# Kernel optimization log

Measured on AMD Instinct MI355X. Metric: run time of the kernel, lower is better.

## Reference

```python
import jax, jax.numpy as jnp
import numpy as np

N, E = 50000, 800000
IN_C, HID, OUT_C, HEADS = 768, 64, 8, 8
NEG_SLOPE = 0.2
BN_EPS = 1e-5


def _bn(x, g, b, m, v):
    # BatchNorm1d in eval mode with running stats
    return (x - m) * jax.lax.rsqrt(v + BN_EPS) * g + b


def _gat_conv(x, W, att_src, att_dst, bias, src, dst, n):
    H, C = att_src.shape
    xw = (x @ W).reshape(n, H, C)                      # [N,H,C]
    a_src = jnp.sum(xw * att_src, axis=-1)             # [N,H]
    a_dst = jnp.sum(xw * att_dst, axis=-1)             # [N,H]
    alpha = jax.nn.leaky_relu(a_src[src] + a_dst[dst], NEG_SLOPE)  # [E',H]
    amax = jax.ops.segment_max(alpha, dst, num_segments=n)          # [N,H]
    ex = jnp.exp(alpha - amax[dst])
    denom = jax.ops.segment_sum(ex, dst, num_segments=n)            # [N,H]
    coef = ex / denom[dst]                                          # [E',H]
    out = jax.ops.segment_sum(xw[src] * coef[:, :, None], dst, num_segments=n)
    return out.reshape(n, H * C) + bias


def setup_inputs() -> dict:
    key = jax.random.key(0)
    ks = jax.random.split(key, 24)
    d = {}
    d['x'] = jax.random.normal(ks[0], (N, IN_C), dtype=jnp.float32)
    d['edge_index'] = jax.random.randint(ks[1], (2, E), 0, N, dtype=jnp.int32)
    d['proj_W'] = jax.random.normal(ks[2], (IN_C, HID), dtype=jnp.float32) * (IN_C ** -0.5)
    d['proj_b'] = jnp.zeros((HID,), jnp.float32)
    for i, kb in zip((1, 2, 3), (ks[3], ks[4], ks[5])):
        k1, k2 = jax.random.split(kb)
        d[f'bn{i}_g'] = jnp.ones((HID,), jnp.float32)
        d[f'bn{i}_b'] = jnp.zeros((HID,), jnp.float32)
        d[f'bn{i}_m'] = jax.random.normal(k1, (HID,), dtype=jnp.float32) * 0.1
        d[f'bn{i}_v'] = jax.random.uniform(k2, (HID,), dtype=jnp.float32, minval=0.5, maxval=1.5)
    C1 = HID // HEADS
    d['W1'] = jax.random.normal(ks[6], (HID, HEADS * C1), dtype=jnp.float32) * (HID ** -0.5)
    d['att_src1'] = jax.random.normal(ks[7], (HEADS, C1), dtype=jnp.float32) * 0.1
    d['att_dst1'] = jax.random.normal(ks[8], (HEADS, C1), dtype=jnp.float32) * 0.1
    d['b1'] = jnp.zeros((HEADS * C1,), jnp.float32)
    d['W2'] = jax.random.normal(ks[9], (HID, HID), dtype=jnp.float32) * (HID ** -0.5)
    d['att_src2'] = jax.random.normal(ks[10], (1, HID), dtype=jnp.float32) * 0.1
    d['att_dst2'] = jax.random.normal(ks[11], (1, HID), dtype=jnp.float32) * 0.1
    d['b2'] = jnp.zeros((HID,), jnp.float32)
    d['cls_W'] = jax.random.normal(ks[12], (HID, OUT_C), dtype=jnp.float32) * (HID ** -0.5)
    d['cls_b'] = jnp.zeros((OUT_C,), jnp.float32)
    return d


def reference(x, edge_index, proj_W, proj_b,
              bn1_g, bn1_b, bn1_m, bn1_v,
              W1, att_src1, att_dst1, b1,
              bn2_g, bn2_b, bn2_m, bn2_v,
              W2, att_src2, att_dst2, b2,
              bn3_g, bn3_b, bn3_m, bn3_v,
              cls_W, cls_b):
    n = x.shape[0]
    # add self-loops (PyG GATConv default)
    loop = jnp.arange(n, dtype=edge_index.dtype)
    src = jnp.concatenate([edge_index[0], loop])
    dst = jnp.concatenate([edge_index[1], loop])

    h = x @ proj_W + proj_b
    h = jax.nn.elu(_bn(h, bn1_g, bn1_b, bn1_m, bn1_v))
    identity = h
    h = _gat_conv(h, W1, att_src1, att_dst1, b1, src, dst, n)
    h = jax.nn.elu(_bn(h, bn2_g, bn2_b, bn2_m, bn2_v) + identity)
    identity = h
    h = _gat_conv(h, W2, att_src2, att_dst2, b2, src, dst, n)
    h = jax.nn.elu(_bn(h, bn3_g, bn3_b, bn3_m, bn3_v) + identity)
    return h @ cls_W + cls_b
```

## Files before the change

### kernel.cpp

```cpp
#include <hip/hip_runtime.h>

typedef __bf16 bf16;
typedef __attribute__((ext_vector_type(8))) __bf16 bf16x8;
typedef __attribute__((ext_vector_type(4))) __bf16 bf16x4;
typedef __attribute__((ext_vector_type(4))) float f32x4;
typedef unsigned short u16;

#define LSTR  40
#define LSTR2 72
#define BN_EPS 1e-5f

__device__ inline float bfl(unsigned int w) { return __uint_as_float(w << 16); }
__device__ inline float bfh(unsigned int w) { return __uint_as_float(w & 0xffff0000u); }

__global__ __launch_bounds__(256) void k_prep(
        const float* __restrict__ W0, const float* __restrict__ W1, const float* __restrict__ W2,
        bf16* __restrict__ Wt0, bf16* __restrict__ Wt1, bf16* __restrict__ Wt2,
        int* __restrict__ cnt, int n)
{
    int i = blockIdx.x*256 + threadIdx.x;
    const int T = 768*64 + 8192;
    if (i < 768*64)            { int k = i>>6, n_ = i&63;                  Wt0[n_*768+k] = (bf16)W0[i]; }
    else if (i < 768*64+4096)  { int j = i-768*64;      int k=j>>6,c=j&63; Wt1[c*64+k]  = (bf16)W1[j]; }
    else if (i < T)            { int j = i-768*64-4096; int k=j>>6,c=j&63; Wt2[c*64+k]  = (bf16)W2[j]; }
    int j = i - T;
    if (j >= 0 && j < n) cnt[j] = 0;
}

__global__ __launch_bounds__(256) void k_fused_proj(
        const float* __restrict__ A, const bf16* __restrict__ Bt,
        const bf16* __restrict__ W1t, int M,
        const float* __restrict__ pb, const float* __restrict__ g,
        const float* __restrict__ bb, const float* __restrict__ mm, const float* __restrict__ vv,
        const float* __restrict__ att_s, const float* __restrict__ att_d,
        bf16* __restrict__ h0b, bf16* __restrict__ xwb,
        float* __restrict__ a_s, float* __restrict__ a_d)
{
    const int K = 768;
    __shared__ bf16 xs[2][64*LSTR];
    __shared__ bf16 bs[2][64*LSTR];
    __shared__ bf16 hs [64*LSTR2];
    __shared__ bf16 w1s[64*LSTR2];
    __shared__ float sC[64], cC[64];

    int t = threadIdx.x;
    int w = t >> 6, lane = t & 63;
    int q = lane >> 4, l16 = lane & 15;
    int row0 = blockIdx.x * 64;
    int sRow = t >> 2, sK = (t & 3) * 8;

    if (t < 64) {
        float s = rsqrtf(vv[t] + BN_EPS) * g[t];
        sC[t] = s;
        cC[t] = (pb[t] - mm[t]) * s + bb[t];
    }
    {
        int r = t >> 2, c0 = (t & 3) * 16;
        *(bf16x8*)(w1s + r*LSTR2 + c0)     = *(const bf16x8*)(W1t + r*64 + c0);
        *(bf16x8*)(w1s + r*LSTR2 + c0 + 8) = *(const bf16x8*)(W1t + r*64 + c0 + 8);
    }

    auto loadA = [&](int k0) -> bf16x8 {
        bf16x8 xv;
        #pragma unroll
        for (int i = 0; i < 8; ++i) xv[i] = (bf16)0.f;
        int gr = row0 + sRow;
        if (gr < M) {
            const float* ap = A + (size_t)gr*K + k0 + sK;
            float4 f0 = *(const float4*)ap;
            float4 f1 = *(const float4*)(ap + 4);
            xv[0]=(bf16)f0.x; xv[1]=(bf16)f0.y; xv[2]=(bf16)f0.z; xv[3]=(bf16)f0.w;
            xv[4]=(bf16)f1.x; xv[5]=(bf16)f1.y; xv[6]=(bf16)f1.z; xv[7]=(bf16)f1.w;
        }
        return xv;
    };
    auto loadB = [&](int k0) -> bf16x8 {
        return *(const bf16x8*)(Bt + (size_t)sRow*K + k0 + sK);
    };

    f32x4 acc[4];
    #pragma unroll
    for (int i = 0; i < 4; ++i) { acc[i][0]=0.f; acc[i][1]=0.f; acc[i][2]=0.f; acc[i][3]=0.f; }

    bf16x8 xv = loadA(0);
    bf16x8 bv = loadB(0);
    *(bf16x8*)(&xs[0][sRow*LSTR + sK]) = xv;
    *(bf16x8*)(&bs[0][sRow*LSTR + sK]) = bv;
    __syncthreads();

    int cur = 0;
    for (int k0 = 0; k0 < K; k0 += 32) {
        if (k0 + 32 < K) {
            xv = loadA(k0 + 32);
            bv = loadB(k0 + 32);
        }
        bf16x8 af = *(bf16x8*)(&xs[cur][(w*16 + l16)*LSTR + q*8]);
        #pragma unroll
        for (int tt = 0; tt < 4; ++tt) {
            bf16x8 bfr = *(bf16x8*)(&bs[cur][(tt*16 + l16)*LSTR + q*8]);
            acc[tt] = __builtin_amdgcn_mfma_f32_16x16x32_bf16(af, bfr, acc[tt], 0, 0, 0);
        }
        if (k0 + 32 < K) {
            *(bf16x8*)(&xs[cur^1][sRow*LSTR + sK]) = xv;
            *(bf16x8*)(&bs[cur^1][sRow*LSTR + sK]) = bv;
            __syncthreads();
            cur ^= 1;
        }
    }

    #pragma unroll
    for (int tt = 0; tt < 4; ++tt) {
        int col = tt*16 + l16;
        #pragma unroll
        for (int r = 0; r < 4; ++r) {
            int rl = w*16 + q*4 + r;
            float val = acc[tt][r] * sC[col] + cC[col];
            val = val > 0.f ? val : __expf(val) - 1.f;
            hs[rl*LSTR2 + col] = (bf16)val;
            int row = row0 + rl;
            if (row < M) h0b[(size_t)row*64 + col] = (bf16)val;
        }
    }
    __syncthreads();

    f32x4 acc2[4];
    #pragma unroll
    for (int i = 0; i < 4; ++i) { acc2[i][0]=0.f; acc2[i][1]=0.f; acc2[i][2]=0.f; acc2[i][3]=0.f; }
    #pragma unroll
    for (int ks = 0; ks < 2; ++ks) {
        bf16x8 af = *(bf16x8*)(&hs[(w*16 + l16)*LSTR2 + ks*32 + q*8]);
        #pragma unroll
        for (int tt = 0; tt < 4; ++tt) {
            bf16x8 bfr = *(bf16x8*)(&w1s[(tt*16 + l16)*LSTR2 + ks*32 + q*8]);
            acc2[tt] = __builtin_amdgcn_mfma_f32_16x16x32_bf16(af, bfr, acc2[tt], 0, 0, 0);
        }
    }

    #pragma unroll
    for (int tt = 0; tt < 4; ++tt) {
        int col = tt*16 + l16;
        #pragma unroll
        for (int r = 0; r < 4; ++r) {
            int row = row0 + w*16 + q*4 + r;
            if (row < M) xwb[(size_t)row*64 + col] = (bf16)acc2[tt][r];
        }
    }
    #pragma unroll
    for (int r = 0; r < 4; ++r) {
        int row = row0 + w*16 + q*4 + r;
        float ps[4], pd[4];
        #pragma unroll
        for (int tt = 0; tt < 4; ++tt) {
            int col = tt*16 + l16;
            ps[tt] = acc2[tt][r] * att_s[col];
            pd[tt] = acc2[tt][r] * att_d[col];
        }
        #pragma unroll
        for (int off = 1; off < 8; off <<= 1) {
            #pragma unroll
            for (int tt = 0; tt < 4; ++tt) {
                ps[tt] += __shfl_xor(ps[tt], off);
                pd[tt] += __shfl_xor(pd[tt], off);
            }
        }
        if ((l16 & 7) == 0 && row < M) {
            int hb = l16 >> 3;
            #pragma unroll
            for (int tt = 0; tt < 4; ++tt) {
                a_s[row*8 + 2*tt + hb] = ps[tt];
                a_d[row*8 + 2*tt + hb] = pd[tt];
            }
        }
    }
}

template<int MODE, bool ABF, int H>
__global__ __launch_bounds__(256) void k_gemm64(
        const void* __restrict__ Av, const bf16* __restrict__ Bt, int M, int K,
        const float* __restrict__ pb, const float* __restrict__ g, const float* __restrict__ bb,
        const float* __restrict__ mm, const float* __restrict__ vv,
        bf16* __restrict__ outB,
        float* __restrict__ a_s, float* __restrict__ a_d,
        const float* __restrict__ att_s, const float* __restrict__ att_d)
{
    __shared__ bf16 xs[64*LSTR];
    __shared__ bf16 bs[64*LSTR];
    __shared__ float sC[64], cC[64];

    int t = threadIdx.x;
    int w = t >> 6, lane = t & 63;
    int q = lane >> 4, l16 = lane & 15;
    int row0 = blockIdx.x * 64;
    int sRow = t >> 2, sK = (t & 3) * 8;

    auto loadA = [&](int k0) -> bf16x8 {
        bf16x8 xv;
        #pragma unroll
        for (int i = 0; i < 8; ++i) xv[i] = (bf16)0.f;
        int gr = row0 + sRow;
        if (gr < M) {
            if constexpr (ABF) {
                xv = *(const bf16x8*)((const bf16*)Av + (size_t)gr*K + k0 + sK);
            } else {
                const float* ap = (const float*)Av + (size_t)gr*K + k0 + sK;
                float4 f0 = *(const float4*)ap;
                float4 f1 = *(const float4*)(ap + 4);
                xv[0]=(bf16)f0.x; xv[1]=(bf16)f0.y; xv[2]=(bf16)f0.z; xv[3]=(bf16)f0.w;
                xv[4]=(bf16)f1.x; xv[5]=(bf16)f1.y; xv[6]=(bf16)f1.z; xv[7]=(bf16)f1.w;
            }
        }
        return xv;
    };
    auto loadB = [&](int k0) -> bf16x8 {
        return *(const bf16x8*)(Bt + (size_t)sRow*K + k0 + sK);
    };

    f32x4 acc[4];
    #pragma unroll
    for (int i = 0; i < 4; ++i) { acc[i][0]=0.f; acc[i][1]=0.f; acc[i][2]=0.f; acc[i][3]=0.f; }

    bf16x8 xv = loadA(0);
    bf16x8 bv = loadB(0);

    for (int k0 = 0; k0 < K; k0 += 32) {
        *(bf16x8*)(xs + sRow*LSTR + sK) = xv;
        *(bf16x8*)(bs + sRow*LSTR + sK) = bv;
        __syncthreads();
        if (k0 + 32 < K) {
            xv = loadA(k0 + 32);
            bv = loadB(k0 + 32);
        }
        bf16x8 af = *(bf16x8*)(xs + (w*16 + l16)*LSTR + q*8);
        #pragma unroll
        for (int tt = 0; tt < 4; ++tt) {
            bf16x8 bfr = *(bf16x8*)(bs + (tt*16 + l16)*LSTR + q*8);
            acc[tt] = __builtin_amdgcn_mfma_f32_16x16x32_bf16(af, bfr, acc[tt], 0, 0, 0);
        }
        __syncthreads();
    }

    if constexpr (MODE == 0) {
        if (t < 64) {
            float s = rsqrtf(vv[t] + BN_EPS) * g[t];
            sC[t] = s;
            cC[t] = (pb[t] - mm[t]) * s + bb[t];
        }
        __syncthreads();
    }

    #pragma unroll
    for (int tt = 0; tt < 4; ++tt) {
        int col = tt*16 + l16;
        #pragma unroll
        for (int r = 0; r < 4; ++r) {
            int row = row0 + w*16 + q*4 + r;
            if (row < M) {
                float val = acc[tt][r];
                if constexpr (MODE == 0) {
                    val = val * sC[col] + cC[col];
                    val = val > 0.f ? val : __expf(val) - 1.f;
                }
                outB[(size_t)row*64 + col] = (bf16)val;
            }
        }
    }

    if constexpr (MODE == 1) {
        #pragma unroll
        for (int r = 0; r < 4; ++r) {
            int row = row0 + w*16 + q*4 + r;
            if constexpr (H == 1) {
                float ps = 0.f, pd = 0.f;
                #pragma unroll
                for (int tt = 0; tt < 4; ++tt) {
                    int col = tt*16 + l16;
                    ps += acc[tt][r] * att_s[col];
                    pd += acc[tt][r] * att_d[col];
                }
                #pragma unroll
                for (int off = 1; off < 16; off <<= 1) {
                    ps += __shfl_xor(ps, off);
                    pd += __shfl_xor(pd, off);
                }
                if (l16 == 0 && row < M) { a_s[row] = ps; a_d[row] = pd; }
            } else {
                float ps[4], pd[4];
                #pragma unroll
                for (int tt = 0; tt < 4; ++tt) {
                    int col = tt*16 + l16;
                    ps[tt] = acc[tt][r] * att_s[col];
                    pd[tt] = acc[tt][r] * att_d[col];
                }
                #pragma unroll
                for (int off = 1; off < 8; off <<= 1) {
                    #pragma unroll
                    for (int tt = 0; tt < 4; ++tt) {
                        ps[tt] += __shfl_xor(ps[tt], off);
                        pd[tt] += __shfl_xor(pd[tt], off);
                    }
                }
                if ((l16 & 7) == 0 && row < M) {
                    int hb = l16 >> 3;
                    #pragma unroll
                    for (int tt = 0; tt < 4; ++tt) {
                        a_s[row*8 + 2*tt + hb] = ps[tt];
                        a_d[row*8 + 2*tt + hb] = pd[tt];
                    }
                }
            }
        }
    }
}

__global__ __launch_bounds__(256) void k_count(const int* __restrict__ dst, int E, int* cnt) {
    int i = blockIdx.x*256 + threadIdx.x;
    if (i < E) atomicAdd(&cnt[dst[i]], 1);
}
__global__ __launch_bounds__(256) void k_scan_block(const int* __restrict__ cnt,
        int* __restrict__ rp, int* __restrict__ bsum, int n) {
    __shared__ int s[256];
    int t = threadIdx.x, v = blockIdx.x*256 + t;
    int x = (v < n) ? cnt[v] : 0;
    s[t] = x; __syncthreads();
    for (int off = 1; off < 256; off <<= 1) {
        int y = (t >= off) ? s[t-off] : 0;
        __syncthreads();
        s[t] += y;
        __syncthreads();
    }
    if (v < n) rp[v+1] = s[t];
    if (t == 255) bsum[blockIdx.x] = s[255];
}
__global__ __launch_bounds__(256) void k_finalize(int* __restrict__ rp, const int* __restrict__ bsum,
        const int* __restrict__ cnt, int* __restrict__ cursor, int n, int nb) {
    __shared__ int s[256];
    int t = threadIdx.x;
    int x = (t < nb) ? bsum[t] : 0;
    s[t] = x; __syncthreads();
    for (int off = 1; off < 256; off <<= 1) {
        int y = (t >= off) ? s[t-off] : 0;
        __syncthreads();
        s[t] += y;
        __syncthreads();
    }
    int v = blockIdx.x*256 + t;
    if (v < n) {
        int b = v >> 8;
        int off0 = (b == 0) ? 0 : s[b-1];
        int val = rp[v+1] + off0;
        rp[v+1] = val;
        cursor[v] = val - cnt[v];
        if (v == 0) rp[0] = 0;
    }
}
__global__ __launch_bounds__(256) void k_scatter(const int* __restrict__ src, const int* __restrict__ dst,
        int E, int* __restrict__ cursor, u16* __restrict__ in_src) {
    int i = blockIdx.x*256 + threadIdx.x;
    if (i < E) {
        int pos = atomicAdd(&cursor[dst[i]], 1);
        in_src[pos] = (u16)src[i];
    }
}

template<int H, bool CLS>
__global__ __launch_bounds__(256) void k_gat_agg(const bf16* __restrict__ xwb,
        const float* __restrict__ a_src, const float* __restrict__ a_dst,
        const int* __restrict__ rp, const u16* __restrict__ in_src,
        const float* __restrict__ bias,
        const float* __restrict__ g_, const float* __restrict__ bb,
        const float* __restrict__ mm, const float* __restrict__ vv,
        const bf16* __restrict__ resid, bf16* __restrict__ outB, float* __restrict__ outF,
        const float* __restrict__ clsW, const float* __restrict__ clsb, int n)
{
    int wv = (blockIdx.x*256 + threadIdx.x) >> 6;
    int lane = threadIdx.x & 63;
    if (wv >= n) return;
    int eg = lane >> 4;
    int s  = lane & 15;
    int c0 = s * 4;
    int h  = (H == 8) ? (s >> 1) : 0;
    float adst = a_dst[(size_t)wv*H + h];

    float a0 = 0.f, a1 = 0.f, a2 = 0.f, a3 = 0.f, den = 0.f;

    if (eg == 0) {
        float asf = a_src[(size_t)wv*H + h] + adst;
        asf = (asf > 0.f) ? asf : 0.2f*asf;
        float ex = __expf(asf);
        uint2 xw = *(const uint2*)(xwb + (size_t)wv*64 + c0);
        a0 = ex*bfl(xw.x); a1 = ex*bfh(xw.x); a2 = ex*bfl(xw.y); a3 = ex*bfh(xw.y);
        den = ex;
    }

    int beg = rp[wv], end = rp[wv+1];
    int e = beg;
    for (; e + 8 <= end; e += 8) {
        int u0 = (int)in_src[e + eg];
        int u1 = (int)in_src[e + 4 + eg];
        float s0 = a_src[(size_t)u0*H + h];
        float s1 = a_src[(size_t)u1*H + h];
        uint2 x0 = *(const uint2*)(xwb + (size_t)u0*64 + c0);
        uint2 x1 = *(const uint2*)(xwb + (size_t)u1*64 + c0);
        float al0 = s0 + adst; al0 = (al0 > 0.f) ? al0 : 0.2f*al0;
        float al1 = s1 + adst; al1 = (al1 > 0.f) ? al1 : 0.2f*al1;
        float e0 = __expf(al0), e1 = __expf(al1);
        a0 += e0*bfl(x0.x) + e1*bfl(x1.x);
        a1 += e0*bfh(x0.x) + e1*bfh(x1.x);
        a2 += e0*bfl(x0.y) + e1*bfl(x1.y);
        a3 += e0*bfh(x0.y) + e1*bfh(x1.y);
        den += e0 + e1;
    }
    for (; e < end; e += 4) {
        int idx = e + eg;
        bool act = idx < end;
        int u = act ? (int)in_src[idx] : 0;
        float sv = a_src[(size_t)u*H + h];
        uint2 xw = *(const uint2*)(xwb + (size_t)u*64 + c0);
        float al = sv + adst; al = (al > 0.f) ? al : 0.2f*al;
        float ex = act ? __expf(al) : 0.f;
        a0 += ex*bfl(xw.x); a1 += ex*bfh(xw.x); a2 += ex*bfl(xw.y); a3 += ex*bfh(xw.y);
        den += ex;
    }

    #pragma unroll
    for (int off = 16; off < 64; off <<= 1) {
        a0 += __shfl_xor(a0, off);
        a1 += __shfl_xor(a1, off);
        a2 += __shfl_xor(a2, off);
        a3 += __shfl_xor(a3, off);
        den += __shfl_xor(den, off);
    }

    float inv = 1.f / den;
    uint2 rz = *(const uint2*)(resid + (size_t)wv*64 + c0);
    float v[4]  = { a0*inv, a1*inv, a2*inv, a3*inv };
    float rv[4] = { bfl(rz.x), bfh(rz.x), bfl(rz.y), bfh(rz.y) };
    #pragma unroll
    for (int j = 0; j < 4; ++j) {
        int c = c0 + j;
        float val = v[j] + bias[c];
        float sc = rsqrtf(vv[c] + BN_EPS) * g_[c];
        val = (val - mm[c]) * sc + bb[c];
        val += rv[j];
        val = (val > 0.f) ? val : __expf(val) - 1.f;
        v[j] = val;
    }

    if constexpr (!CLS) {
        if (eg == 0) {
            bf16x4 o;
            o[0] = (bf16)v[0]; o[1] = (bf16)v[1]; o[2] = (bf16)v[2]; o[3] = (bf16)v[3];
            *(bf16x4*)(outB + (size_t)wv*64 + c0) = o;
        }
    } else {
        if (eg != 0) { v[0] = 0.f; v[1] = 0.f; v[2] = 0.f; v[3] = 0.f; }
        float p[8];
        #pragma unroll
        for (int o = 0; o < 8; ++o) {
            p[o] = v[0]*clsW[(c0+0)*8+o] + v[1]*clsW[(c0+1)*8+o]
                 + v[2]*clsW[(c0+2)*8+o] + v[3]*clsW[(c0+3)*8+o];
        }
        #pragma unroll
        for (int off = 1; off < 64; off <<= 1) {
            #pragma unroll
            for (int o = 0; o < 8; ++o) p[o] += __shfl_xor(p[o], off);
        }
        if (lane < 8) {
            float r = 0.f;
            #pragma unroll
            for (int o = 0; o < 8; ++o) if (lane == o) r = p[o] + clsb[o];
            outF[(size_t)wv*8 + lane] = r;
        }
    }
}

extern "C" void kernel_launch(void* const* d_in, const int* in_sizes, int n_in,
                              void* d_out, int out_size, void* d_ws, size_t ws_size,
                              hipStream_t stream)
{
    const float* x      = (const float*)d_in[0];
    const int*   ei     = (const int*)  d_in[1];
    const float* proj_W = (const float*)d_in[2];
    const float* proj_b = (const float*)d_in[3];
    const float* bn1_g  = (const float*)d_in[4];
    const float* bn1_b  = (const float*)d_in[5];
    const float* bn1_m  = (const float*)d_in[6];
    const float* bn1_v  = (const float*)d_in[7];
    const float* bn2_g  = (const float*)d_in[8];
    const float* bn2_b  = (const float*)d_in[9];
    const float* bn2_m  = (const float*)d_in[10];
    const float* bn2_v  = (const float*)d_in[11];
    const float* bn3_g  = (const float*)d_in[12];
    const float* bn3_b  = (const float*)d_in[13];
    const float* bn3_m  = (const float*)d_in[14];
    const float* bn3_v  = (const float*)d_in[15];
    const float* W1     = (const float*)d_in[16];
    const float* att_s1 = (const float*)d_in[17];
    const float* att_d1 = (const float*)d_in[18];
    const float* b1     = (const float*)d_in[19];
    const float* W2     = (const float*)d_in[20];
    const float* att_s2 = (const float*)d_in[21];
    const float* att_d2 = (const float*)d_in[22];
    const float* b2     = (const float*)d_in[23];
    const float* cls_W  = (const float*)d_in[24];
    const float* cls_b  = (const float*)d_in[25];

    const int N = in_sizes[0] / 768;
    const int E = in_sizes[1] / 2;
    const int* srce = ei;
    const int* dste = ei + E;

    char* p = (char*)d_ws;
    auto carve = [&](size_t bytes) -> void* {
        void* r = (void*)p;
        p += (bytes + 255) & ~(size_t)255;
        return r;
    };
    bf16*  Wt0    = (bf16*) carve((size_t)64*768*2);
    bf16*  Wt1    = (bf16*) carve((size_t)64*64*2);
    bf16*  Wt2    = (bf16*) carve((size_t)64*64*2);
    bf16*  h0b    = (bf16*) carve((size_t)N*64*2);
    bf16*  h1b    = (bf16*) carve((size_t)N*64*2);
    bf16*  xwb    = (bf16*) carve((size_t)N*64*2);
    float* a_s    = (float*)carve((size_t)N*8*4);
    float* a_d    = (float*)carve((size_t)N*8*4);
    int*   cnt    = (int*)  carve((size_t)N*4);
    int*   rp     = (int*)  carve((size_t)(N+1)*4);
    int*   cursor = (int*)  carve((size_t)N*4);
    int*   bsum   = (int*)  carve(1024);
    u16*   in_src = (u16*)  carve((size_t)E*2);

    const int nb = (N + 255) / 256;
    const int PREP = 768*64 + 8192;

    k_prep<<<(PREP + N + 255)/256, 256, 0, stream>>>(proj_W, W1, W2, Wt0, Wt1, Wt2, cnt, N);

    k_count<<<(E + 255)/256, 256, 0, stream>>>(dste, E, cnt);
    k_scan_block<<<nb, 256, 0, stream>>>(cnt, rp, bsum, N);
    k_finalize<<<nb, 256, 0, stream>>>(rp, bsum, cnt, cursor, N, nb);
    k_scatter<<<(E + 255)/256, 256, 0, stream>>>(srce, dste, E, cursor, in_src);

    k_fused_proj<<<(N + 63)/64, 256, 0, stream>>>(x, Wt0, Wt1, N,
            proj_b, bn1_g, bn1_b, bn1_m, bn1_v, att_s1, att_d1,
            h0b, xwb, a_s, a_d);

    k_gat_agg<8, false><<<(N + 3)/4, 256, 0, stream>>>(xwb, a_s, a_d, rp, in_src,
            b1, bn2_g, bn2_b, bn2_m, bn2_v, h0b, h1b, nullptr, nullptr, nullptr, N);

    k_gemm64<1, true, 1><<<(N + 63)/64, 256, 0, stream>>>(h1b, Wt2, N, 64,
            nullptr, nullptr, nullptr, nullptr, nullptr, xwb, a_s, a_d, att_s2, att_d2);
    k_gat_agg<1, true><<<(N + 3)/4, 256, 0, stream>>>(xwb, a_s, a_d, rp, in_src,
            b2, bn3_g, bn3_b, bn3_m, bn3_v, h1b, nullptr, (float*)d_out, cls_W, cls_b, N);
}
```

Baseline: 482.8 us.

## Merge CSR build into cooperative kernel and fuse layer-2 projection into aggregation

Replaces the separate weight-prep, count, scan, finalize and scatter kernels with one cooperative kernel using grid-wide syncs. Removes the separate layer-2 GEMM by computing h1·W2 and the attention logits inside the first aggregation kernel, using wave shuffles with W2 staged in shared memory. This cuts kernel launches and the round trip of h1 through memory, but each 4-node block now reloads the full 64x64 fp32 W2 into shared memory. Grid syncs also serialize the CSR build.

```diff
diff --git a/kernel.cpp b/kernel.cpp
--- a/kernel.cpp
+++ b/kernel.cpp
@@ -1,4 +1,7 @@
 #include <hip/hip_runtime.h>
+#include <hip/hip_cooperative_groups.h>
+
+namespace cg = cooperative_groups;
 
 typedef __bf16 bf16;
 typedef __attribute__((ext_vector_type(8))) __bf16 bf16x8;
@@ -13,18 +16,72 @@
 __device__ inline float bfl(unsigned int w) { return __uint_as_float(w << 16); }
 __device__ inline float bfh(unsigned int w) { return __uint_as_float(w & 0xffff0000u); }
 
-__global__ __launch_bounds__(256) void k_prep(
-        const float* __restrict__ W0, const float* __restrict__ W1, const float* __restrict__ W2,
-        bf16* __restrict__ Wt0, bf16* __restrict__ Wt1, bf16* __restrict__ Wt2,
-        int* __restrict__ cnt, int n)
+__global__ __launch_bounds__(256) void k_csr(
+        const float* __restrict__ W0, const float* __restrict__ W1,
+        bf16* __restrict__ Wt0, bf16* __restrict__ Wt1,
+        const int* __restrict__ src, const int* __restrict__ dst, int E, int n,
+        int* __restrict__ cnt, int* __restrict__ rp, int* __restrict__ cursor,
+        int* __restrict__ bsum, u16* __restrict__ in_src)
 {
-    int i = blockIdx.x*256 + threadIdx.x;
-    const int T = 768*64 + 8192;
-    if (i < 768*64)            { int k = i>>6, n_ = i&63;                  Wt0[n_*768+k] = (bf16)W0[i]; }
-    else if (i < 768*64+4096)  { int j = i-768*64;      int k=j>>6,c=j&63; Wt1[c*64+k]  = (bf16)W1[j]; }
-    else if (i < T)            { int j = i-768*64-4096; int k=j>>6,c=j&63; Wt2[c*64+k]  = (bf16)W2[j]; }
-    int j = i - T;
-    if (j >= 0 && j < n) cnt[j] = 0;
+    cg::grid_group grid = cg::this_grid();
+    const int tid = blockIdx.x*256 + threadIdx.x;
+    const int nth = gridDim.x*256;
+    __shared__ int s[256];
+
+    const int T = 768*64 + 4096;
+    for (int i = tid; i < T; i += nth) {
+        if (i < 768*64) { int k = i>>6, n_ = i&63;            Wt0[n_*768+k] = (bf16)W0[i]; }
+        else            { int j = i-768*64; int k=j>>6,c=j&63; Wt1[c*64+k]  = (bf16)W1[j]; }
+    }
+    for (int i = tid; i < n; i += nth) cnt[i] = 0;
+    grid.sync();
+
+    for (int i = tid; i < E; i += nth) atomicAdd(&cnt[dst[i]], 1);
+    grid.sync();
+
+    const int nchunk = (n + 255) >> 8;
+    for (int c = blockIdx.x; c < nchunk; c += gridDim.x) {
+        int t = threadIdx.x, v = c*256 + t;
+        int x = (v < n) ? cnt[v] : 0;
+        s[t] = x; __syncthreads();
+        for (int off = 1; off < 256; off <<= 1) {
+            int y = (t >= off) ? s[t-off] : 0;
+            __syncthreads();
+            s[t] += y;
+            __syncthreads();
+        }
+        if (v < n) rp[v+1] = s[t];
+        if (t == 255) bsum[c] = s[255];
+        __syncthreads();
+    }
+    grid.sync();
+
+    if (blockIdx.x == 0) {
+        int t = threadIdx.x;
+        int x = (t < nchunk) ? bsum[t] : 0;
+        s[t] = x; __syncthreads();
+        for (int off = 1; off < 256; off <<= 1) {
+            int y = (t >= off) ? s[t-off] : 0;
+            __syncthreads();
+            s[t] += y;
+            __syncthreads();
+        }
+        if (t < nchunk) bsum[t] = s[t] - x;
+    }
+    grid.sync();
+
+    for (int v = tid; v < n; v += nth) {
+        int val = rp[v+1] + bsum[v >> 8];
+        rp[v+1] = val;
+        cursor[v] = val - cnt[v];
+    }
+    if (tid == 0) rp[0] = 0;
+    grid.sync();
+
+    for (int i = tid; i < E; i += nth) {
+        int pos = atomicAdd(&cursor[dst[i]], 1);
+        in_src[pos] = (u16)src[i];
+    }
 }
 
 __global__ __launch_bounds__(256) void k_fused_proj(
@@ -174,217 +231,42 @@
     }
 }
 
-template<int MODE, bool ABF, int H>
-__global__ __launch_bounds__(256) void k_gemm64(
-        const void* __restrict__ Av, const bf16* __restrict__ Bt, int M, int K,
-        const float* __restrict__ pb, const float* __restrict__ g, const float* __restrict__ bb,
-        const float* __restrict__ mm, const float* __restrict__ vv,
-        bf16* __restrict__ outB,
-        float* __restrict__ a_s, float* __restrict__ a_d,
-        const float* __restrict__ att_s, const float* __restrict__ att_d)
-{
-    __shared__ bf16 xs[64*LSTR];
-    __shared__ bf16 bs[64*LSTR];
-    __shared__ float sC[64], cC[64];
-
-    int t = threadIdx.x;
-    int w = t >> 6, lane = t & 63;
-    int q = lane >> 4, l16 = lane & 15;
-    int row0 = blockIdx.x * 64;
-    int sRow = t >> 2, sK = (t & 3) * 8;
-
-    auto loadA = [&](int k0) -> bf16x8 {
-        bf16x8 xv;
-        #pragma unroll
-        for (int i = 0; i < 8; ++i) xv[i] = (bf16)0.f;
-        int gr = row0 + sRow;
-        if (gr < M) {
-            if constexpr (ABF) {
-                xv = *(const bf16x8*)((const bf16*)Av + (size_t)gr*K + k0 + sK);
-            } else {
-                const float* ap = (const float*)Av + (size_t)gr*K + k0 + sK;
-                float4 f0 = *(const float4*)ap;
-                float4 f1 = *(const float4*)(ap + 4);
-                xv[0]=(bf16)f0.x; xv[1]=(bf16)f0.y; xv[2]=(bf16)f0.z; xv[3]=(bf16)f0.w;
-                xv[4]=(bf16)f1.x; xv[5]=(bf16)f1.y; xv[6]=(bf16)f1.z; xv[7]=(bf16)f1.w;
-            }
-        }
-        return xv;
-    };
-    auto loadB = [&](int k0) -> bf16x8 {
-        return *(const bf16x8*)(Bt + (size_t)sRow*K + k0 + sK);
-    };
-
-    f32x4 acc[4];
-    #pragma unroll
-    for (int i = 0; i < 4; ++i) { acc[i][0]=0.f; acc[i][1]=0.f; acc[i][2]=0.f; acc[i][3]=0.f; }
-
-    bf16x8 xv = loadA(0);
-    bf16x8 bv = loadB(0);
-
-    for (int k0 = 0; k0 < K; k0 += 32) {
-        *(bf16x8*)(xs + sRow*LSTR + sK) = xv;
-        *(bf16x8*)(bs + sRow*LSTR + sK) = bv;
-        __syncthreads();
-        if (k0 + 32 < K) {
-            xv = loadA(k0 + 32);
-            bv = loadB(k0 + 32);
-        }
-        bf16x8 af = *(bf16x8*)(xs + (w*16 + l16)*LSTR + q*8);
-        #pragma unroll
-        for (int tt = 0; tt < 4; ++tt) {
-            bf16x8 bfr = *(bf16x8*)(bs + (tt*16 + l16)*LSTR + q*8);
-            acc[tt] = __builtin_amdgcn_mfma_f32_16x16x32_bf16(af, bfr, acc[tt], 0, 0, 0);
-        }
-        __syncthreads();
-    }
-
-    if constexpr (MODE == 0) {
-        if (t < 64) {
-            float s = rsqrtf(vv[t] + BN_EPS) * g[t];
-            sC[t] = s;
-            cC[t] = (pb[t] - mm[t]) * s + bb[t];
-        }
-        __syncthreads();
-    }
-
-    #pragma unroll
-    for (int tt = 0; tt < 4; ++tt) {
-        int col = tt*16 + l16;
-        #pragma unroll
-        for (int r = 0; r < 4; ++r) {
-            int row = row0 + w*16 + q*4 + r;
-            if (row < M) {
-                float val = acc[tt][r];
-                if constexpr (MODE == 0) {
-                    val = val * sC[col] + cC[col];
-                    val = val > 0.f ? val : __expf(val) - 1.f;
-                }
-                outB[(size_t)row*64 + col] = (bf16)val;
-            }
-        }
-    }
-
-    if constexpr (MODE == 1) {
-        #pragma unroll
-        for (int r = 0; r < 4; ++r) {
-            int row = row0 + w*16 + q*4 + r;
-            if constexpr (H == 1) {
-                float ps = 0.f, pd = 0.f;
-                #pragma unroll
-                for (int tt = 0; tt < 4; ++tt) {
-                    int col = tt*16 + l16;
-                    ps += acc[tt][r] * att_s[col];
-                    pd += acc[tt][r] * att_d[col];
-                }
-                #pragma unroll
-                for (int off = 1; off < 16; off <<= 1) {
-                    ps += __shfl_xor(ps, off);
-                    pd += __shfl_xor(pd, off);
-                }
-                if (l16 == 0 && row < M) { a_s[row] = ps; a_d[row] = pd; }
-            } else {
-                float ps[4], pd[4];
-                #pragma unroll
-                for (int tt = 0; tt < 4; ++tt) {
-                    int col = tt*16 + l16;
-                    ps[tt] = acc[tt][r] * att_s[col];
-                    pd[tt] = acc[tt][r] * att_d[col];
-                }
-                #pragma unroll
-                for (int off = 1; off < 8; off <<= 1) {
-                    #pragma unroll
-                    for (int tt = 0; tt < 4; ++tt) {
-                        ps[tt] += __shfl_xor(ps[tt], off);
-                        pd[tt] += __shfl_xor(pd[tt], off);
-                    }
-                }
-                if ((l16 & 7) == 0 && row < M) {
-                    int hb = l16 >> 3;
-                    #pragma unroll
-                    for (int tt = 0; tt < 4; ++tt) {
-                        a_s[row*8 + 2*tt + hb] = ps[tt];
-                        a_d[row*8 + 2*tt + hb] = pd[tt];
-                    }
-                }
-            }
-        }
-    }
-}
-
-__global__ __launch_bounds__(256) void k_count(const int* __restrict__ dst, int E, int* cnt) {
-    int i = blockIdx.x*256 + threadIdx.x;
-    if (i < E) atomicAdd(&cnt[dst[i]], 1);
-}
-__global__ __launch_bounds__(256) void k_scan_block(const int* __restrict__ cnt,
-        int* __restrict__ rp, int* __restrict__ bsum, int n) {
-    __shared__ int s[256];
-    int t = threadIdx.x, v = blockIdx.x*256 + t;
-    int x = (v < n) ? cnt[v] : 0;
-    s[t] = x; __syncthreads();
-    for (int off = 1; off < 256; off <<= 1) {
-        int y = (t >= off) ? s[t-off] : 0;
-        __syncthreads();
-        s[t] += y;
-        __syncthreads();
-    }
-    if (v < n) rp[v+1] = s[t];
-    if (t == 255) bsum[blockIdx.x] = s[255];
-}
-__global__ __launch_bounds__(256) void k_finalize(int* __restrict__ rp, const int* __restrict__ bsum,
-        const int* __restrict__ cnt, int* __restrict__ cursor, int n, int nb) {
-    __shared__ int s[256];
-    int t = threadIdx.x;
-    int x = (t < nb) ? bsum[t] : 0;
-    s[t] = x; __syncthreads();
-    for (int off = 1; off < 256; off <<= 1) {
-        int y = (t >= off) ? s[t-off] : 0;
-        __syncthreads();
-        s[t] += y;
-        __syncthreads();
-    }
-    int v = blockIdx.x*256 + t;
-    if (v < n) {
-        int b = v >> 8;
-        int off0 = (b == 0) ? 0 : s[b-1];
-        int val = rp[v+1] + off0;
-        rp[v+1] = val;
-        cursor[v] = val - cnt[v];
-        if (v == 0) rp[0] = 0;
-    }
-}
-__global__ __launch_bounds__(256) void k_scatter(const int* __restrict__ src, const int* __restrict__ dst,
-        int E, int* __restrict__ cursor, u16* __restrict__ in_src) {
-    int i = blockIdx.x*256 + threadIdx.x;
-    if (i < E) {
-        int pos = atomicAdd(&cursor[dst[i]], 1);
-        in_src[pos] = (u16)src[i];
-    }
-}
-
-template<int H, bool CLS>
-__global__ __launch_bounds__(256) void k_gat_agg(const bf16* __restrict__ xwb,
-        const float* __restrict__ a_src, const float* __restrict__ a_dst,
+__global__ __launch_bounds__(256) void k_agg1(
+        const bf16* __restrict__ xwb, const float* __restrict__ a_src, const float* __restrict__ a_dst,
         const int* __restrict__ rp, const u16* __restrict__ in_src,
         const float* __restrict__ bias,
         const float* __restrict__ g_, const float* __restrict__ bb,
         const float* __restrict__ mm, const float* __restrict__ vv,
-        const bf16* __restrict__ resid, bf16* __restrict__ outB, float* __restrict__ outF,
-        const float* __restrict__ clsW, const float* __restrict__ clsb, int n)
+        const bf16* __restrict__ resid,
+        const float* __restrict__ W2, const float* __restrict__ att_s, const float* __restrict__ att_d,
+        bf16* __restrict__ h1b, bf16* __restrict__ xw2b,
+        float* __restrict__ a_s2, float* __restrict__ a_d2, int n)
 {
+    __shared__ float w2s[64*68];
+    {
+        int t = threadIdx.x;
+        int row = t >> 2, col0 = (t & 3) * 16;
+        #pragma unroll
+        for (int i = 0; i < 4; ++i) {
+            float4 f = *(const float4*)(W2 + row*64 + col0 + i*4);
+            *(float4*)&w2s[row*68 + col0 + i*4] = f;
+        }
+    }
+    __syncthreads();
+
     int wv = (blockIdx.x*256 + threadIdx.x) >> 6;
     int lane = threadIdx.x & 63;
     if (wv >= n) return;
     int eg = lane >> 4;
     int s  = lane & 15;
     int c0 = s * 4;
-    int h  = (H == 8) ? (s >> 1) : 0;
-    float adst = a_dst[(size_t)wv*H + h];
+    int h  = s >> 1;
+    float adst = a_dst[(size_t)wv*8 + h];
 
     float a0 = 0.f, a1 = 0.f, a2 = 0.f, a3 = 0.f, den = 0.f;
 
     if (eg == 0) {
-        float asf = a_src[(size_t)wv*H + h] + adst;
+        float asf = a_src[(size_t)wv*8 + h] + adst;
         asf = (asf > 0.f) ? asf : 0.2f*asf;
         float ex = __expf(asf);
         uint2 xw = *(const uint2*)(xwb + (size_t)wv*64 + c0);
@@ -397,8 +279,8 @@
     for (; e + 8 <= end; e += 8) {
         int u0 = (int)in_src[e + eg];
         int u1 = (int)in_src[e + 4 + eg];
-        float s0 = a_src[(size_t)u0*H + h];
-        float s1 = a_src[(size_t)u1*H + h];
+        float s0 = a_src[(size_t)u0*8 + h];
+        float s1 = a_src[(size_t)u1*8 + h];
         uint2 x0 = *(const uint2*)(xwb + (size_t)u0*64 + c0);
         uint2 x1 = *(const uint2*)(xwb + (size_t)u1*64 + c0);
         float al0 = s0 + adst; al0 = (al0 > 0.f) ? al0 : 0.2f*al0;
@@ -414,7 +296,7 @@
         int idx = e + eg;
         bool act = idx < end;
         int u = act ? (int)in_src[idx] : 0;
-        float sv = a_src[(size_t)u*H + h];
+        float sv = a_src[(size_t)u*8 + h];
         uint2 xw = *(const uint2*)(xwb + (size_t)u*64 + c0);
         float al = sv + adst; al = (al > 0.f) ? al : 0.2f*al;
         float ex = act ? __expf(al) : 0.f;
@@ -446,31 +328,144 @@
         v[j] = val;
     }
 
-    if constexpr (!CLS) {
-        if (eg == 0) {
-            bf16x4 o;
-            o[0] = (bf16)v[0]; o[1] = (bf16)v[1]; o[2] = (bf16)v[2]; o[3] = (bf16)v[3];
-            *(bf16x4*)(outB + (size_t)wv*64 + c0) = o;
-        }
-    } else {
-        if (eg != 0) { v[0] = 0.f; v[1] = 0.f; v[2] = 0.f; v[3] = 0.f; }
-        float p[8];
-        #pragma unroll
-        for (int o = 0; o < 8; ++o) {
-            p[o] = v[0]*clsW[(c0+0)*8+o] + v[1]*clsW[(c0+1)*8+o]
-                 + v[2]*clsW[(c0+2)*8+o] + v[3]*clsW[(c0+3)*8+o];
-        }
-        #pragma unroll
-        for (int off = 1; off < 64; off <<= 1) {
-            #pragma unroll
-            for (int o = 0; o < 8; ++o) p[o] += __shfl_xor(p[o], off);
-        }
-        if (lane < 8) {
-            float r = 0.f;
-            #pragma unroll
-            for (int o = 0; o < 8; ++o) if (lane == o) r = p[o] + clsb[o];
-            outF[(size_t)wv*8 + lane] = r;
-        }
+    if (eg == 0) {
+        bf16x4 o;
+        o[0] = (bf16)v[0]; o[1] = (bf16)v[1]; o[2] = (bf16)v[2]; o[3] = (bf16)v[3];
+        *(bf16x4*)(h1b + (size_t)wv*64 + c0) = o;
+    }
+
+    float o0 = 0.f, o1 = 0.f, o2 = 0.f, o3 = 0.f;
+    #pragma unroll
+    for (int k = 0; k < 16; ++k) {
+        float h0v = __shfl(v[0], k);
+        float h1v = __shfl(v[1], k);
+        float h2v = __shfl(v[2], k);
+        float h3v = __shfl(v[3], k);
+        f32x4 w0 = *(const f32x4*)&w2s[(4*k+0)*68 + c0];
+        f32x4 w1 = *(const f32x4*)&w2s[(4*k+1)*68 + c0];
+        f32x4 w2 = *(const f32x4*)&w2s[(4*k+2)*68 + c0];
+        f32x4 w3 = *(const f32x4*)&w2s[(4*k+3)*68 + c0];
+        o0 += h0v*w0[0] + h1v*w1[0] + h2v*w2[0] + h3v*w3[0];
+        o1 += h0v*w0[1] + h1v*w1[1] + h2v*w2[1] + h3v*w3[1];
+        o2 += h0v*w0[2] + h1v*w1[2] + h2v*w2[2] + h3v*w3[2];
+        o3 += h0v*w0[3] + h1v*w1[3] + h2v*w2[3] + h3v*w3[3];
+    }
+
+    if (eg == 0) {
+        bf16x4 o;
+        o[0] = (bf16)o0; o[1] = (bf16)o1; o[2] = (bf16)o2; o[3] = (bf16)o3;
+        *(bf16x4*)(xw2b + (size_t)wv*64 + c0) = o;
+    }
+
+    float ps = o0*att_s[c0] + o1*att_s[c0+1] + o2*att_s[c0+2] + o3*att_s[c0+3];
+    float pd = o0*att_d[c0] + o1*att_d[c0+1] + o2*att_d[c0+2] + o3*att_d[c0+3];
+    #pragma unroll
+    for (int off = 1; off < 16; off <<= 1) {
+        ps += __shfl_xor(ps, off);
+        pd += __shfl_xor(pd, off);
+    }
+    if (lane == 0) { a_s2[wv] = ps; a_d2[wv] = pd; }
+}
+
+__global__ __launch_bounds__(256) void k_agg2(const bf16* __restrict__ xwb,
+        const float* __restrict__ a_src, const float* __restrict__ a_dst,
+        const int* __restrict__ rp, const u16* __restrict__ in_src,
+        const float* __restrict__ bias,
+        const float* __restrict__ g_, const float* __restrict__ bb,
+        const float* __restrict__ mm, const float* __restrict__ vv,
+        const bf16* __restrict__ resid, float* __restrict__ outF,
+        const float* __restrict__ clsW, const float* __restrict__ clsb, int n)
+{
+    int wv = (blockIdx.x*256 + threadIdx.x) >> 6;
+    int lane = threadIdx.x & 63;
+    if (wv >= n) return;
+    int eg = lane >> 4;
+    int s  = lane & 15;
+    int c0 = s * 4;
+    float adst = a_dst[wv];
+
+    float a0 = 0.f, a1 = 0.f, a2 = 0.f, a3 = 0.f, den = 0.f;
+
+    if (eg == 0) {
+        float asf = a_src[wv] + adst;
+        asf = (asf > 0.f) ? asf : 0.2f*asf;
+        float ex = __expf(asf);
+        uint2 xw = *(const uint2*)(xwb + (size_t)wv*64 + c0);
+        a0 = ex*bfl(xw.x); a1 = ex*bfh(xw.x); a2 = ex*bfl(xw.y); a3 = ex*bfh(xw.y);
+        den = ex;
+    }
+
+    int beg = rp[wv], end = rp[wv+1];
+    int e = beg;
+    for (; e + 8 <= end; e += 8) {
+        int u0 = (int)in_src[e + eg];
+        int u1 = (int)in_src[e + 4 + eg];
+        float s0 = a_src[u0];
+        float s1 = a_src[u1];
+        uint2 x0 = *(const uint2*)(xwb + (size_t)u0*64 + c0);
+        uint2 x1 = *(const uint2*)(xwb + (size_t)u1*64 + c0);
+        float al0 = s0 + adst; al0 = (al0 > 0.f) ? al0 : 0.2f*al0;
+        float al1 = s1 + adst; al1 = (al1 > 0.f) ? al1 : 0.2f*al1;
+        float e0 = __expf(al0), e1 = __expf(al1);
+        a0 += e0*bfl(x0.x) + e1*bfl(x1.x);
+        a1 += e0*bfh(x0.x) + e1*bfh(x1.x);
+        a2 += e0*bfl(x0.y) + e1*bfl(x1.y);
+        a3 += e0*bfh(x0.y) + e1*bfh(x1.y);
+        den += e0 + e1;
+    }
+    for (; e < end; e += 4) {
+        int idx = e + eg;
+        bool act = idx < end;
+        int u = act ? (int)in_src[idx] : 0;
+        float sv = a_src[u];
+        uint2 xw = *(const uint2*)(xwb + (size_t)u*64 + c0);
+        float al = sv + adst; al = (al > 0.f) ? al : 0.2f*al;
+        float ex = act ? __expf(al) : 0.f;
+        a0 += ex*bfl(xw.x); a1 += ex*bfh(xw.x); a2 += ex*bfl(xw.y); a3 += ex*bfh(xw.y);
+        den += ex;
+    }
+
+    #pragma unroll
+    for (int off = 16; off < 64; off <<= 1) {
+        a0 += __shfl_xor(a0, off);
+        a1 += __shfl_xor(a1, off);
+        a2 += __shfl_xor(a2, off);
+        a3 += __shfl_xor(a3, off);
+        den += __shfl_xor(den, off);
+    }
+
+    float inv = 1.f / den;
+    uint2 rz = *(const uint2*)(resid + (size_t)wv*64 + c0);
+    float v[4]  = { a0*inv, a1*inv, a2*inv, a3*inv };
+    float rv[4] = { bfl(rz.x), bfh(rz.x), bfl(rz.y), bfh(rz.y) };
+    #pragma unroll
+    for (int j = 0; j < 4; ++j) {
+        int c = c0 + j;
+        float val = v[j] + bias[c];
+        float sc = rsqrtf(vv[c] + BN_EPS) * g_[c];
+        val = (val - mm[c]) * sc + bb[c];
+        val += rv[j];
+        val = (val > 0.f) ? val : __expf(val) - 1.f;
+        v[j] = val;
+    }
+
+    if (eg != 0) { v[0] = 0.f; v[1] = 0.f; v[2] = 0.f; v[3] = 0.f; }
+    float p[8];
+    #pragma unroll
+    for (int o = 0; o < 8; ++o) {
+        p[o] = v[0]*clsW[(c0+0)*8+o] + v[1]*clsW[(c0+1)*8+o]
+             + v[2]*clsW[(c0+2)*8+o] + v[3]*clsW[(c0+3)*8+o];
+    }
+    #pragma unroll
+    for (int off = 1; off < 64; off <<= 1) {
+        #pragma unroll
+        for (int o = 0; o < 8; ++o) p[o] += __shfl_xor(p[o], off);
+    }
+    if (lane < 8) {
+        float r = 0.f;
+        #pragma unroll
+        for (int o = 0; o < 8; ++o) if (lane == o) r = p[o] + clsb[o];
+        outF[(size_t)wv*8 + lane] = r;
     }
 }
 
@@ -505,8 +500,8 @@
     const float* cls_W  = (const float*)d_in[24];
     const float* cls_b  = (const float*)d_in[25];
 
-    const int N = in_sizes[0] / 768;
-    const int E = in_sizes[1] / 2;
+    int N = in_sizes[0] / 768;
+    int E = in_sizes[1] / 2;
     const int* srce = ei;
     const int* dste = ei + E;
 
@@ -518,37 +513,35 @@
     };
     bf16*  Wt0    = (bf16*) carve((size_t)64*768*2);
     bf16*  Wt1    = (bf16*) carve((size_t)64*64*2);
-    bf16*  Wt2    = (bf16*) carve((size_t)64*64*2);
     bf16*  h0b    = (bf16*) carve((size_t)N*64*2);
     bf16*  h1b    = (bf16*) carve((size_t)N*64*2);
     bf16*  xwb    = (bf16*) carve((size_t)N*64*2);
+    bf16*  xw2b   = (bf16*) carve((size_t)N*64*2);
     float* a_s    = (float*)carve((size_t)N*8*4);
     float* a_d    = (float*)carve((size_t)N*8*4);
+    float* a_s2   = (float*)carve((size_t)N*4);
+    float* a_d2   = (float*)carve((size_t)N*4);
     int*   cnt    = (int*)  carve((size_t)N*4);
     int*   rp     = (int*)  carve((size_t)(N+1)*4);
     int*   cursor = (int*)  carve((size_t)N*4);
     int*   bsum   = (int*)  carve(1024);
     u16*   in_src = (u16*)  carve((size_t)E*2);
 
-    const int nb = (N + 255) / 256;
-    const int PREP = 768*64 + 8192;
-
-    k_prep<<<(PREP + N + 255)/256, 256, 0, stream>>>(proj_W, W1, W2, Wt0, Wt1, Wt2, cnt, N);
-
-    k_count<<<(E + 255)/256, 256, 0, stream>>>(dste, E, cnt);
-    k_scan_block<<<nb, 256, 0, stream>>>(cnt, rp, bsum, N);
-    k_finalize<<<nb, 256, 0, stream>>>(rp, bsum, cnt, cursor, N, nb);
-    k_scatter<<<(E + 255)/256, 256, 0, stream>>>(srce, dste, E, cursor, in_src);
+    {
+        void* args[] = { (void*)&proj_W, (void*)&W1, (void*)&Wt0, (void*)&Wt1,
+                         (void*)&srce, (void*)&dste, (void*)&E, (void*)&N,
+                         (void*)&cnt, (void*)&rp, (void*)&cursor, (void*)&bsum, (void*)&in_src };
+        hipLaunchCooperativeKernel((const void*)k_csr, dim3(512), dim3(256), args, 0, stream);
+    }
 
     k_fused_proj<<<(N + 63)/64, 256, 0, stream>>>(x, Wt0, Wt1, N,
             proj_b, bn1_g, bn1_b, bn1_m, bn1_v, att_s1, att_d1,
             h0b, xwb, a_s, a_d);
 
-    k_gat_agg<8, false><<<(N + 3)/4, 256, 0, stream>>>(xwb, a_s, a_d, rp, in_src,
-            b1, bn2_g, bn2_b, bn2_m, bn2_v, h0b, h1b, nullptr, nullptr, nullptr, N);
-
-    k_gemm64<1, true, 1><<<(N + 63)/64, 256, 0, stream>>>(h1b, Wt2, N, 64,
-            nullptr, nullptr, nullptr, nullptr, nullptr, xwb, a_s, a_d, att_s2, att_d2);
-    k_gat_agg<1, true><<<(N + 3)/4, 256, 0, stream>>>(xwb, a_s, a_d, rp, in_src,
-            b2, bn3_g, bn3_b, bn3_m, bn3_v, h1b, nullptr, (float*)d_out, cls_W, cls_b, N);
+    k_agg1<<<(N + 3)/4, 256, 0, stream>>>(xwb, a_s, a_d, rp, in_src,
+            b1, bn2_g, bn2_b, bn2_m, bn2_v, h0b,
+            W2, att_s2, att_d2, h1b, xw2b, a_s2, a_d2, N);
+
+    k_agg2<<<(N + 3)/4, 256, 0, stream>>>(xw2b, a_s2, a_d2, rp, in_src,
+            b2, bn3_g, bn3_b, bn3_m, bn3_v, h1b, (float*)d_out, cls_W, cls_b, N);
 }
```

Result: slower. 842.4 us (+74.5%).
